# Optimization experiments

Hardware: AMD Instinct MI355X
Metric: run time of the kernel (lower is better)

Reference implementation:

```python
import jax, jax.numpy as jnp
import numpy as np

IN_FEATURES = 1024
OUT_FEATURES = 1024
N_TOKENS = 32768


def setup_inputs() -> dict:
    key = jax.random.key(0)
    kx, kw, kb = jax.random.split(key, 3)
    x = jax.random.normal(kx, (N_TOKENS, IN_FEATURES), dtype=jnp.float32)
    weight = jax.random.normal(kw, (OUT_FEATURES, IN_FEATURES), dtype=jnp.float32)
    bias = jax.random.normal(kb, (OUT_FEATURES,), dtype=jnp.float32)
    return {"x": x, "weight": weight, "bias": bias}


def reference(x, weight, bias):
    # Binarize weights to {-1, 0, +1} via sign (matches torch.sign semantics),
    # then dense linear: y = x @ sign(W)^T + b
    bw = jnp.sign(weight)  # [out, in]
    return jnp.einsum('ni,oi->no', x, bw) + bias
```

## Files before the change

kernel.cpp:

```cpp
#include <hip/hip_runtime.h>
#include <stdint.h>

#define M_TOK 32768
#define N_OUT 1024
#define K_IN  1024

#define BM 128
#define BN 128
#define BK 32

typedef __bf16 bf16_t;
typedef bf16_t bf16x8 __attribute__((ext_vector_type(8)));
typedef float  floatx4 __attribute__((ext_vector_type(4)));

__device__ __forceinline__ unsigned short f2bf(float f) {
    uint32_t u = __float_as_uint(f);
    u += 0x7FFFu + ((u >> 16) & 1u);
    return (unsigned short)(u >> 16);
}

__global__ void cvt_x_kernel(const float* __restrict__ x, unsigned short* __restrict__ xb) {
    size_t i = (size_t)blockIdx.x * blockDim.x + threadIdx.x;
    const float4* xv = (const float4*)(x + i * 8);
    float4 a = xv[0];
    float4 b = xv[1];
    unsigned int p0 = (unsigned int)f2bf(a.x) | ((unsigned int)f2bf(a.y) << 16);
    unsigned int p1 = (unsigned int)f2bf(a.z) | ((unsigned int)f2bf(a.w) << 16);
    unsigned int p2 = (unsigned int)f2bf(b.x) | ((unsigned int)f2bf(b.y) << 16);
    unsigned int p3 = (unsigned int)f2bf(b.z) | ((unsigned int)f2bf(b.w) << 16);
    uint4 o; o.x = p0; o.y = p1; o.z = p2; o.w = p3;
    *(uint4*)(xb + i * 8) = o;
}

__global__ void cvt_w_kernel(const float* __restrict__ w, unsigned short* __restrict__ wb) {
    size_t i = (size_t)blockIdx.x * blockDim.x + threadIdx.x;
    const float4* wv = (const float4*)(w + i * 4);
    float4 a = wv[0];
    unsigned short s0 = (a.x > 0.f) ? 0x3F80u : ((a.x < 0.f) ? 0xBF80u : 0u);
    unsigned short s1 = (a.y > 0.f) ? 0x3F80u : ((a.y < 0.f) ? 0xBF80u : 0u);
    unsigned short s2 = (a.z > 0.f) ? 0x3F80u : ((a.z < 0.f) ? 0xBF80u : 0u);
    unsigned short s3 = (a.w > 0.f) ? 0x3F80u : ((a.w < 0.f) ? 0xBF80u : 0u);
    uint2 o;
    o.x = (unsigned int)s0 | ((unsigned int)s1 << 16);
    o.y = (unsigned int)s2 | ((unsigned int)s3 << 16);
    *(uint2*)(wb + i * 4) = o;
}

__global__ __launch_bounds__(256) void gemm_sign_kernel(
    const unsigned short* __restrict__ A,
    const unsigned short* __restrict__ B,
    const float* __restrict__ bias,
    float* __restrict__ C)
{
    __shared__ __align__(16) unsigned short sA[BM * BK];
    __shared__ __align__(16) unsigned short sB[BN * BK];

    const int t    = threadIdx.x;
    const int bn   = blockIdx.x;
    const int bm   = blockIdx.y;
    const int wave = t >> 6;
    const int lane = t & 63;
    const int wm   = wave >> 1;
    const int wn   = wave & 1;
    const int lrow = lane & 15;
    const int quad = lane >> 4;

    const int row0 = t >> 2;
    const int col0 = (t & 3) * 8;

    const size_t a_base0 = (size_t)(bm * BM + row0) * K_IN + col0;
    const size_t a_base1 = (size_t)(bm * BM + 64 + row0) * K_IN + col0;
    const size_t b_base0 = (size_t)(bn * BN + row0) * K_IN + col0;
    const size_t b_base1 = (size_t)(bn * BN + 64 + row0) * K_IN + col0;

    floatx4 acc[4][4] = {};

    for (int kt = 0; kt < K_IN / BK; ++kt) {
        const int kbase = kt * BK;
        uint4 a0 = *(const uint4*)(A + a_base0 + kbase);
        uint4 a1 = *(const uint4*)(A + a_base1 + kbase);
        uint4 b0 = *(const uint4*)(B + b_base0 + kbase);
        uint4 b1 = *(const uint4*)(B + b_base1 + kbase);

        __syncthreads();
        *(uint4*)(sA + row0 * BK + col0)        = a0;
        *(uint4*)(sA + (64 + row0) * BK + col0) = a1;
        *(uint4*)(sB + row0 * BK + col0)        = b0;
        *(uint4*)(sB + (64 + row0) * BK + col0) = b1;
        __syncthreads();

        bf16x8 af[4], bfr[4];
#pragma unroll
        for (int i = 0; i < 4; ++i)
            af[i] = *(const bf16x8*)(sA + (wm * 64 + i * 16 + lrow) * BK + quad * 8);
#pragma unroll
        for (int j = 0; j < 4; ++j)
            bfr[j] = *(const bf16x8*)(sB + (wn * 64 + j * 16 + lrow) * BK + quad * 8);

#pragma unroll
        for (int i = 0; i < 4; ++i)
#pragma unroll
            for (int j = 0; j < 4; ++j)
                acc[i][j] = __builtin_amdgcn_mfma_f32_16x16x32_bf16(af[i], bfr[j], acc[i][j], 0, 0, 0);
    }

    const int crow_base = bm * BM + wm * 64;
    const int ccol_base = bn * BN + wn * 64;
#pragma unroll
    for (int j = 0; j < 4; ++j) {
        const int col = ccol_base + j * 16 + lrow;
        const float bv = bias[col];
#pragma unroll
        for (int i = 0; i < 4; ++i) {
            const int rbase = crow_base + i * 16 + quad * 4;
#pragma unroll
            for (int r = 0; r < 4; ++r) {
                C[(size_t)(rbase + r) * N_OUT + col] = acc[i][j][r] + bv;
            }
        }
    }
}

extern "C" void kernel_launch(void* const* d_in, const int* in_sizes, int n_in,
                              void* d_out, int out_size, void* d_ws, size_t ws_size,
                              hipStream_t stream) {
    const float* x    = (const float*)d_in[0];
    const float* w    = (const float*)d_in[1];
    const float* bias = (const float*)d_in[2];
    float* out        = (float*)d_out;

    unsigned short* xb = (unsigned short*)d_ws;
    unsigned short* wb = (unsigned short*)((char*)d_ws + (size_t)M_TOK * K_IN * 2);

    cvt_x_kernel<<<16384, 256, 0, stream>>>(x, xb);
    cvt_w_kernel<<<1024, 256, 0, stream>>>(w, wb);

    dim3 grid(N_OUT / BN, M_TOK / BM);
    gemm_sign_kernel<<<grid, 256, 0, stream>>>(xb, wb, bias, out);
}
```

Measured before the change: 337.0 us.

## Stage GEMM tiles with direct global-to-LDS loads and swizzle block order

```diff
diff --git a/kernel.cpp b/kernel.cpp
--- a/kernel.cpp
+++ b/kernel.cpp
@@ -46,6 +46,13 @@
     *(uint2*)(wb + i * 4) = o;
 }
 
+__device__ __forceinline__ void stage16(const unsigned short* gsrc, unsigned short* ldst) {
+    __builtin_amdgcn_global_load_lds(
+        (const __attribute__((address_space(1))) unsigned int*)gsrc,
+        (__attribute__((address_space(3))) unsigned int*)ldst,
+        16, 0, 0);
+}
+
 __global__ __launch_bounds__(256) void gemm_sign_kernel(
     const unsigned short* __restrict__ A,
     const unsigned short* __restrict__ B,
@@ -56,8 +63,10 @@
     __shared__ __align__(16) unsigned short sB[BN * BK];
 
     const int t    = threadIdx.x;
-    const int bn   = blockIdx.x;
-    const int bm   = blockIdx.y;
+    const int b    = blockIdx.x;
+    const int bm   = ((b >> 6) << 3) + (b & 7);
+    const int bn   = (b >> 3) & 7;
+
     const int wave = t >> 6;
     const int lane = t & 63;
     const int wm   = wave >> 1;
@@ -65,28 +74,29 @@
     const int lrow = lane & 15;
     const int quad = lane >> 4;
 
-    const int row0 = t >> 2;
-    const int col0 = (t & 3) * 8;
+    const int srow = (wave << 5) + (lane >> 2);
+    const int scol = (lane & 3) << 3;
+    const int lds_off = (t << 3);
 
-    const size_t a_base0 = (size_t)(bm * BM + row0) * K_IN + col0;
-    const size_t a_base1 = (size_t)(bm * BM + 64 + row0) * K_IN + col0;
-    const size_t b_base0 = (size_t)(bn * BN + row0) * K_IN + col0;
-    const size_t b_base1 = (size_t)(bn * BN + 64 + row0) * K_IN + col0;
+    unsigned short* sA0 = sA + wave * 1024 + lane * 8;
+    unsigned short* sA1 = sA + wave * 1024 + 512 + lane * 8;
+    unsigned short* sB0 = sB + wave * 1024 + lane * 8;
+    unsigned short* sB1 = sB + wave * 1024 + 512 + lane * 8;
+
+    const unsigned short* gA0 = A + (size_t)(bm * BM + srow)      * K_IN + scol;
+    const unsigned short* gA1 = A + (size_t)(bm * BM + srow + 16) * K_IN + scol;
+    const unsigned short* gB0 = B + (size_t)(bn * BN + srow)      * K_IN + scol;
+    const unsigned short* gB1 = B + (size_t)(bn * BN + srow + 16) * K_IN + scol;
 
     floatx4 acc[4][4] = {};
 
     for (int kt = 0; kt < K_IN / BK; ++kt) {
         const int kbase = kt * BK;
-        uint4 a0 = *(const uint4*)(A + a_base0 + kbase);
-        uint4 a1 = *(const uint4*)(A + a_base1 + kbase);
-        uint4 b0 = *(const uint4*)(B + b_base0 + kbase);
-        uint4 b1 = *(const uint4*)(B + b_base1 + kbase);
-
         __syncthreads();
-        *(uint4*)(sA + row0 * BK + col0)        = a0;
-        *(uint4*)(sA + (64 + row0) * BK + col0) = a1;
-        *(uint4*)(sB + row0 * BK + col0)        = b0;
-        *(uint4*)(sB + (64 + row0) * BK + col0) = b1;
+        stage16(gA0 + kbase, sA0);
+        stage16(gA1 + kbase, sA1);
+        stage16(gB0 + kbase, sB0);
+        stage16(gB1 + kbase, sB1);
         __syncthreads();
 
         bf16x8 af[4], bfr[4];
@@ -135,6 +145,5 @@
     cvt_x_kernel<<<16384, 256, 0, stream>>>(x, xb);
     cvt_w_kernel<<<1024, 256, 0, stream>>>(w, wb);
 
-    dim3 grid(N_OUT / BN, M_TOK / BM);
-    gemm_sign_kernel<<<grid, 256, 0, stream>>>(xb, wb, bias, out);
+    gemm_sign_kernel<<<(M_TOK / BM) * (N_OUT / BN), 256, 0, stream>>>(xb, wb, bias, out);
 }
```

Result: faster. 306.8 us (-8.9%).
